# Optimization experiments

Measured on AMD Instinct MI355X. Metric: run time of the kernel, lower is better.

The kernel has to match this reference:

```python
import jax, jax.numpy as jnp
import numpy as np
import math

B, S, E, R = 128, 16, 512, 500  # batch, seq_len, emb_size, relation_num


def setup_inputs() -> dict:
    key = jax.random.key(0)
    ks = jax.random.split(key, 12)
    s = 1.0 / math.sqrt(E)
    emb = jax.random.normal(ks[0], (R + 1, E), jnp.float32) * s
    emb = emb.at[R].set(0.0)  # padding_idx row is zero in torch
    w_ih = jax.random.normal(ks[1], (4 * E, E), jnp.float32) * s
    w_hh = jax.random.normal(ks[2], (4 * E, E), jnp.float32) * s
    b_ih = jax.random.normal(ks[3], (4 * E,), jnp.float32) * s
    b_hh = jax.random.normal(ks[4], (4 * E,), jnp.float32) * s
    fc_w = jax.random.normal(ks[5], (1, E), jnp.float32) * s
    fc_b = jax.random.normal(ks[6], (1,), jnp.float32) * s
    fcq_w = jax.random.normal(ks[7], (E, E), jnp.float32) * s
    fcq_b = jax.random.normal(ks[8], (E,), jnp.float32) * s
    fck_w = jax.random.normal(ks[9], (E, E), jnp.float32) * s
    fck_b = jax.random.normal(ks[10], (E,), jnp.float32) * s
    tokens = jax.random.randint(ks[11], (B, S), 0, R)  # avoid padding idx R
    return dict(tokens=tokens, emb=emb, w_ih=w_ih, w_hh=w_hh, b_ih=b_ih,
                b_hh=b_hh, fc_w=fc_w, fc_b=fc_b, fcq_w=fcq_w, fcq_b=fcq_b,
                fck_w=fck_w, fck_b=fck_b)


def _lstm_pair(x, w_ih, w_hh, b):
    # x: [..., 2, E]; 2-step LSTM from zero state, return final hidden [..., E]
    def cell(xt, h, c):
        g = xt @ w_ih.T + h @ w_hh.T + b
        i, f, gg, o = jnp.split(g, 4, axis=-1)  # torch gate order i,f,g,o
        c = jax.nn.sigmoid(f) * c + jax.nn.sigmoid(i) * jnp.tanh(gg)
        return jax.nn.sigmoid(o) * jnp.tanh(c), c
    z = jnp.zeros_like(x[..., 0, :])
    h1, c1 = cell(x[..., 0, :], z, z)
    h2, _ = cell(x[..., 1, :], h1, c1)
    return h2


def _attention(x, rel_emb, fcq_w, fcq_b, fck_w, fck_b):
    # x: [B,q,E]; keys = [relation embeddings ; x] -> scores [B,q,R+q]
    b = x.shape[0]
    rel = jnp.broadcast_to(rel_emb[None], (b,) + rel_emb.shape)
    kin = jnp.concatenate([rel, x], axis=1)
    k = kin @ fck_w.T + fck_b
    q = x @ fcq_w.T + fcq_b
    return jnp.einsum('bqe,bke->bqk', q, k) / math.sqrt(E)


def _entropy(scores):
    lp = jax.nn.log_softmax(scores, axis=-1)
    return -jnp.sum(jnp.exp(lp) * lp, axis=-1)


def reference(tokens, emb, w_ih, w_hh, b_ih, b_hh, fc_w, fc_b,
              fcq_w, fcq_b, fck_w, fck_b):
    b_lstm = b_ih + b_hh
    rel_emb = emb[:R]  # relation embeddings used as attention keys/values
    cur = emb[tokens]  # [B,S,E]
    bidx = jnp.arange(B)
    losses = []
    for L in range(S, 1, -1):  # lengths processed: S, S-1, ..., 2
        if L > 2:
            # all adjacent pairs, batched 2-step LSTM: [B, L-1, E]
            pairs = jnp.stack([cur[:, :-1], cur[:, 1:]], axis=2)
            h = _lstm_pair(pairs, w_ih, w_hh, b_lstm)
            sc = jax.nn.sigmoid(h @ fc_w.T + fc_b)[..., 0]  # [B, L-1]
            sel = jnp.argmax(sc, axis=-1)  # [B]
            selected = jnp.take_along_axis(h, sel[:, None, None], axis=1)  # [B,1,E]
            scores = _attention(selected, rel_emb, fcq_w, fcq_b, fck_w, fck_b)
            losses.append(_entropy(scores))  # [B,1]
            # weightedAverage: mask is all-False for seq_len==1, plain softmax
            prob = jax.nn.softmax(scores, axis=-1)  # [B,1,R+1]
            all_emb = jnp.concatenate(
                [jnp.broadcast_to(rel_emb[None], (B, R, E)), selected], axis=1)
            merged = jnp.einsum('bqk,bke->bqe', prob, all_emb)[:, 0]  # [B,E]
            # output = inputs.detach().clone(); write merged at sel; drop row sel+1
            base = jax.lax.stop_gradient(cur)
            base = base.at[bidx, sel].set(merged)
            j = jnp.arange(L - 1)[None, :]
            src = j + (j > sel[:, None]).astype(j.dtype)
            cur = jnp.take_along_axis(base, src[:, :, None], axis=1)  # [B,L-1,E]
        else:  # L == 2: plain LSTM over the two tokens
            h = _lstm_pair(cur, w_ih, w_hh, b_lstm)  # [B,E]
            cur = h[:, None, :]
            losses.append(jnp.zeros((B, 1), cur.dtype))
    scores_f = _attention(cur, rel_emb, fcq_w, fcq_b, fck_w, fck_b)  # [B,1,R+1]
    losses.append(_entropy(scores_f))
    loss_tensor = jnp.concatenate(losses, axis=-1)  # [B,S]
    return scores_f[:, 0], loss_tensor
```

## Files before the change

### kernel.cpp

```cpp
#include <hip/hip_runtime.h>
#include <hip/hip_bf16.h>

#define BB 128
#define SS 16
#define EE 512
#define RR 500
#define G4 2048
#define OUT0 64128
#define NSC 501
#define NPAIR 2047
#define NSU 1012

__device__ __forceinline__ float sigm(float x) { return 1.f / (1.f + expf(-x)); }

__device__ float g_blstm[G4];
__device__ float g_blstmr[G4];
__device__ float g_wihr[G4 * EE];
__device__ float g_whhr[G4 * EE];
__device__ float g_fcw[EE + 4];
__device__ float g_qbias[1024];
__device__ float g_Krel[RR * EE];
__device__ float g_cur[BB * SS * EE];
__device__ float g_G[BB * SS * G4];
__device__ float g_h1[BB * SS * EE];
__device__ float g_c1[BB * SS * EE];
__device__ float g_h2[BB * SS * EE];
__device__ float g_sc[BB * SS];
__device__ float g_ent[BB * SS];
__device__ int   g_sel[BB];
__device__ int   g_ord[BB * SS];
__device__ float g_fckwT[EE * EE];
__device__ float g_W2[RR * EE];
__device__ float g_Mx[EE * EE];
__device__ float g_c2[RR + 4];
__device__ float g_v1[EE];
__device__ float g_c0[1];
__device__ float g_su[BB * NSU];

__global__ void k_prep(const float* __restrict__ bih, const float* __restrict__ bhh,
                       const float* __restrict__ fcwv, const float* __restrict__ fcbv,
                       const float* __restrict__ fcqb, const float* __restrict__ fckb) {
    int i = blockIdx.x * blockDim.x + threadIdx.x;
    if (i < G4) g_blstm[i] = bih[i] + bhh[i];
    if (i < EE) {
        g_fcw[i] = fcwv[i];
        g_qbias[i] = fcqb[i];
        g_qbias[EE + i] = fckb[i];
    }
    if (i == 0) g_fcw[EE] = fcbv[0];
    if (i < BB * SS) g_ord[i] = i;
}

__global__ void k_reord(const float* __restrict__ wih, const float* __restrict__ whh) {
    int i = blockIdx.x * blockDim.x + threadIdx.x;
    if (i >= G4 * EE) return;
    int n = i >> 9;
    int k = i & (EE - 1);
    int e = n & (EE - 1);
    int gate = n >> 9;
    int np = 4 * e + gate;
    g_wihr[(size_t)np * EE + k] = wih[i];
    g_whhr[(size_t)np * EE + k] = whh[i];
    if (k == 0) g_blstmr[np] = g_blstm[n];
}

__global__ void k_gather(const int* __restrict__ tok, const float* __restrict__ emb) {
    int i = blockIdx.x * blockDim.x + threadIdx.x;
    if (i >= BB * SS * EE) return;
    int e = i & (EE - 1);
    int r = i >> 9;
    int t = tok[r];
    g_cur[i] = emb[(size_t)t * EE + e];
}

__global__ void k_tr(const float* __restrict__ fckw) {
    int i = blockIdx.x * blockDim.x + threadIdx.x;
    if (i >= EE * EE) return;
    int ep = i >> 9;
    int f = i & (EE - 1);
    g_fckwT[(size_t)f * EE + ep] = fckw[(size_t)ep * EE + f];
}

__global__ __launch_bounds__(512) void k_vprep(const float* __restrict__ fcqw, const float* __restrict__ fckw) {
    __shared__ float sh[512];
    int t = threadIdx.x;
    int blk = blockIdx.x;
    if (blk == 0) {
        float acc = 0.f;
        for (int ep = 0; ep < EE; ep++)
            acc += g_qbias[ep] * fckw[(size_t)ep * EE + t] + g_qbias[EE + ep] * fcqw[(size_t)ep * EE + t];
        g_v1[t] = acc;
    } else if (blk == 1) {
        sh[t] = g_qbias[t] * g_qbias[EE + t];
        __syncthreads();
        for (int s = 256; s > 0; s >>= 1) { if (t < s) sh[t] += sh[t + s]; __syncthreads(); }
        if (t == 0) g_c0[0] = sh[0];
    } else {
        int k = blk - 2;
        sh[t] = g_Krel[(size_t)k * EE + t] * g_qbias[t];
        __syncthreads();
        for (int s = 256; s > 0; s >>= 1) { if (t < s) sh[t] += sh[t + s]; __syncthreads(); }
        if (t == 0) g_c2[k] = sh[0];
    }
}

#define TM 32
#define TN 64
#define TK 32
__device__ __forceinline__ void gemm_dev(
    const float* __restrict__ A, int lda,
    const float* __restrict__ W, int ldw, int wtrans,
    const float* __restrict__ bias, const float* __restrict__ Dadd, int ldd,
    float* __restrict__ C, int ldc, int M, int N, int K)
{
    __shared__ __align__(16) float As[TK][TM + 2];
    __shared__ __align__(16) float Ws[TK][TN + 4];
    int tid = threadIdx.x;
    int mt = blockIdx.y * TM;
    int nt = blockIdx.x * TN;
    int tr = tid >> 4;
    int tc = tid & 15;
    float acc[2][4] = {{0.f,0.f,0.f,0.f},{0.f,0.f,0.f,0.f}};

    int ea = tid * 4;
    int ra = ea >> 5;
    int ka = ea & 31;
    int gmA = mt + ra;
    bool rokA = gmA < M;
    int ew = tid * 8;
    int rw = ew >> 5;
    int kw = ew & 31;
    int gnW = nt + rw;
    bool rokW = gnW < N;

    for (int kt = 0; kt < K; kt += TK) {
        #pragma unroll
        for (int i = 0; i < 4; i++) {
            int gk = kt + ka + i;
            float v = 0.f;
            if (rokA && gk < K) v = A[(size_t)gmA * lda + gk];
            As[ka + i][ra] = v;
        }
        #pragma unroll
        for (int i = 0; i < 8; i++) {
            int gk = kt + kw + i;
            float v = 0.f;
            if (rokW && gk < K)
                v = wtrans ? W[(size_t)gk * ldw + gnW] : W[(size_t)gnW * ldw + gk];
            Ws[kw + i][rw] = v;
        }
        __syncthreads();
        #pragma unroll
        for (int kk = 0; kk < TK; kk++) {
            const float2 a = *(const float2*)&As[kk][2 * tr];
            const float4 w = *(const float4*)&Ws[kk][4 * tc];
            acc[0][0] += a.x * w.x; acc[0][1] += a.x * w.y; acc[0][2] += a.x * w.z; acc[0][3] += a.x * w.w;
            acc[1][0] += a.y * w.x; acc[1][1] += a.y * w.y; acc[1][2] += a.y * w.z; acc[1][3] += a.y * w.w;
        }
        __syncthreads();
    }
    #pragma unroll
    for (int i = 0; i < 2; i++) {
        int gm = mt + 2 * tr + i;
        if (gm >= M) continue;
        #pragma unroll
        for (int j = 0; j < 4; j++) {
            int gn = nt + 4 * tc + j;
            if (gn >= N) continue;
            float v = (i == 0) ? ((j == 0) ? acc[0][0] : (j == 1) ? acc[0][1] : (j == 2) ? acc[0][2] : acc[0][3])
                               : ((j == 0) ? acc[1][0] : (j == 1) ? acc[1][1] : (j == 2) ? acc[1][2] : acc[1][3]);
            if (bias) v += bias[gn];
            if (Dadd) v += Dadd[(size_t)gm * ldd + gn];
            C[(size_t)gm * ldc + gn] = v;
        }
    }
}

#define UM 128
#define UN 128
#define UK 32
template<int MODE>
__global__ __launch_bounds__(256) void kg_bigF() {
    __shared__ __align__(16) float As[UK][UM + 4];
    __shared__ __align__(16) float Ws[UK][UN + 4];
    const float* __restrict__ A = (MODE == 0) ? g_cur : g_h1;
    const float* __restrict__ W = (MODE == 0) ? g_wihr : g_whhr;
    const int M = (MODE == 0) ? (BB * SS) : NPAIR;
    int tid = threadIdx.x;
    int mt = blockIdx.y * UM;
    int nt = blockIdx.x * UN;
    int tr = tid >> 4;
    int tc = tid & 15;
    float acc[8][8] = {};

    int ra = tid & 127;
    int ka = (tid >> 7) << 4;
    int gmA = mt + ra;
    bool rokA = gmA < M;
    const float* Arow = A + (size_t)(rokA ? gmA : 0) * EE;
    const float* Wrow = W + (size_t)(nt + ra) * EE;

    float4 pa[4] = {{0,0,0,0},{0,0,0,0},{0,0,0,0},{0,0,0,0}};
    float4 pw[4];
    #pragma unroll
    for (int j = 0; j < 4; j++) {
        if (rokA) pa[j] = *(const float4*)&Arow[ka + 4 * j];
        pw[j] = *(const float4*)&Wrow[ka + 4 * j];
    }

    for (int kt = 0; kt < EE; kt += UK) {
        __syncthreads();
        #pragma unroll
        for (int j = 0; j < 4; j++) {
            As[ka + 4 * j + 0][ra] = pa[j].x;
            As[ka + 4 * j + 1][ra] = pa[j].y;
            As[ka + 4 * j + 2][ra] = pa[j].z;
            As[ka + 4 * j + 3][ra] = pa[j].w;
            Ws[ka + 4 * j + 0][ra] = pw[j].x;
            Ws[ka + 4 * j + 1][ra] = pw[j].y;
            Ws[ka + 4 * j + 2][ra] = pw[j].z;
            Ws[ka + 4 * j + 3][ra] = pw[j].w;
        }
        __syncthreads();
        if (kt + UK < EE) {
            int k2 = kt + UK + ka;
            #pragma unroll
            for (int j = 0; j < 4; j++) {
                if (rokA) pa[j] = *(const float4*)&Arow[k2 + 4 * j];
                pw[j] = *(const float4*)&Wrow[k2 + 4 * j];
            }
        }
        #pragma unroll
        for (int kk = 0; kk < UK; kk++) {
            const float4 aA = *(const float4*)&As[kk][4 * tr];
            const float4 aB = *(const float4*)&As[kk][64 + 4 * tr];
            const float4 wA = *(const float4*)&Ws[kk][4 * tc];
            const float4 wB = *(const float4*)&Ws[kk][64 + 4 * tc];
            const float am[8] = {aA.x, aA.y, aA.z, aA.w, aB.x, aB.y, aB.z, aB.w};
            const float wn[8] = {wA.x, wA.y, wA.z, wA.w, wB.x, wB.y, wB.z, wB.w};
            #pragma unroll
            for (int i = 0; i < 8; i++)
                #pragma unroll
                for (int j = 0; j < 8; j++)
                    acc[i][j] += am[i] * wn[j];
        }
    }

    int c0 = nt + 4 * tc;
    int c1c = c0 + 64;
    int e0 = (nt >> 2) + tc;
    #pragma unroll
    for (int ri = 0; ri < 8; ri++) {
        int row = (ri < 4) ? (4 * tr + ri) : (60 + 4 * tr + ri);
        int gm = mt + row;
        if (gm >= M) continue;
        float q0x = acc[ri][0], q0y = acc[ri][1], q0z = acc[ri][2], q0w = acc[ri][3];
        float q1x = acc[ri][4], q1y = acc[ri][5], q1z = acc[ri][6], q1w = acc[ri][7];
        if (MODE == 0) {
            const float4 b0 = *(const float4*)&g_blstmr[c0];
            const float4 b1 = *(const float4*)&g_blstmr[c1c];
            q0x += b0.x; q0y += b0.y; q0z += b0.z; q0w += b0.w;
            q1x += b1.x; q1y += b1.y; q1z += b1.z; q1w += b1.w;
            float4 o0 = {q0x, q0y, q0z, q0w};
            float4 o1 = {q1x, q1y, q1z, q1w};
            *(float4*)&g_G[(size_t)gm * G4 + c0]  = o0;
            *(float4*)&g_G[(size_t)gm * G4 + c1c] = o1;
            float cA = sigm(q0x) * tanhf(q0z);
            g_c1[(size_t)gm * EE + e0] = cA;
            g_h1[(size_t)gm * EE + e0] = sigm(q0w) * tanhf(cA);
            float cB = sigm(q1x) * tanhf(q1z);
            g_c1[(size_t)gm * EE + e0 + 16] = cB;
            g_h1[(size_t)gm * EE + e0 + 16] = sigm(q1w) * tanhf(cB);
        } else {
            const float4 d0 = *(const float4*)&g_G[(size_t)(gm + 1) * G4 + c0];
            const float4 d1 = *(const float4*)&g_G[(size_t)(gm + 1) * G4 + c1c];
            q0x += d0.x; q0y += d0.y; q0z += d0.z; q0w += d0.w;
            q1x += d1.x; q1y += d1.y; q1z += d1.z; q1w += d1.w;
            float c1a = g_c1[(size_t)gm * EE + e0];
            float c1b = g_c1[(size_t)gm * EE + e0 + 16];
            float cA = sigm(q0y) * c1a + sigm(q0x) * tanhf(q0z);
            g_h2[(size_t)gm * EE + e0] = sigm(q0w) * tanhf(cA);
            float cB = sigm(q1y) * c1b + sigm(q1x) * tanhf(q1z);
            g_h2[(size_t)gm * EE + e0 + 16] = sigm(q1w) * tanhf(cB);
        }
    }
}

__global__ __launch_bounds__(256) void kg_Krel(const float* __restrict__ emb, const float* __restrict__ fckw) {
    gemm_dev(emb, EE, fckw, EE, 0, g_qbias + EE, nullptr, 0, g_Krel, EE, RR, EE, EE);
}
__global__ __launch_bounds__(256) void kg_W2(const float* __restrict__ fcqw) {
    gemm_dev(g_Krel, EE, fcqw, EE, 1, nullptr, nullptr, 0, g_W2, EE, RR, EE, EE);
}
__global__ __launch_bounds__(256) void kg_Mx(const float* __restrict__ fcqw) {
    gemm_dev(g_fckwT, EE, fcqw, EE, 1, nullptr, nullptr, 0, g_Mx, EE, EE, EE, EE);
}

__global__ __launch_bounds__(256) void k_scI() {
    int m = blockIdx.x;
    int t = threadIdx.x;
    __shared__ float red[256];
    const float* h = g_h2 + (size_t)m * EE;
    float part = h[t] * g_fcw[t] + h[t + 256] * g_fcw[t + 256];
    red[t] = part;
    __syncthreads();
    for (int s = 128; s > 0; s >>= 1) { if (t < s) red[t] += red[t + s]; __syncthreads(); }
    if (t == 0) g_sc[m] = red[0];
}

__global__ __launch_bounds__(256) void k_scP(int L) {
    int m = blockIdx.x;
    int b = m >> 1;
    int tcand = m & 1;
    int s = g_sel[b];
    int p = s - 1 + tcand;
    bool valid = tcand == 0 ? (s >= 1) : (s <= L - 3);
    if (!valid) return;
    int physL = g_ord[b * SS + p];
    int t = threadIdx.x;
    __shared__ float red[256];
    const float* h = g_h2 + (size_t)physL * EE;
    float part = h[t] * g_fcw[t] + h[t + 256] * g_fcw[t + 256];
    red[t] = part;
    __syncthreads();
    for (int s2 = 128; s2 > 0; s2 >>= 1) { if (t < s2) red[t] += red[t + s2]; __syncthreads(); }
    if (t == 0) g_sc[b * SS + p] = red[0];
}

__global__ __launch_bounds__(256) void kg_su(int P) {
    __shared__ __align__(16) float As[TK][TM + 2];
    __shared__ __align__(16) float Ws[TK][TN + 4];
    __shared__ int s_phys[TM];
    int tid = threadIdx.x;
    int mt = blockIdx.y * TM;
    int nt = blockIdx.x * TN;
    int tr = tid >> 4;
    int tc = tid & 15;
    float acc[2][4] = {{0.f,0.f,0.f,0.f},{0.f,0.f,0.f,0.f}};

    if (tid < TM) {
        int b = mt + tid;
        float best = -1e30f; int bi = 0;
        for (int p = 0; p < P; p++) {
            float v = g_sc[b * SS + p];
            if (v > best) { best = v; bi = p; }
        }
        s_phys[tid] = g_ord[b * SS + bi];
        if (blockIdx.x == 0) g_sel[b] = bi;
    }
    __syncthreads();

    int ea = tid * 4;
    int ra = ea >> 5;
    int ka = ea & 31;
    int physA = s_phys[ra];
    int ew = tid * 8;
    int rw = ew >> 5;
    int kw = ew & 31;
    int gnW = nt + rw;
    bool rokW = gnW < NSU;
    const float* Wrow = nullptr;
    if (rokW) Wrow = (gnW < RR) ? (g_W2 + (size_t)gnW * EE) : (g_Mx + (size_t)(gnW - RR) * EE);

    for (int kt = 0; kt < EE; kt += TK) {
        #pragma unroll
        for (int i = 0; i < 4; i++)
            As[ka + i][ra] = g_h2[(size_t)physA * EE + kt + ka + i];
        #pragma unroll
        for (int i = 0; i < 8; i++)
            Ws[kw + i][rw] = rokW ? Wrow[kt + kw + i] : 0.f;
        __syncthreads();
        #pragma unroll
        for (int kk = 0; kk < TK; kk++) {
            const float2 a = *(const float2*)&As[kk][2 * tr];
            const float4 w = *(const float4*)&Ws[kk][4 * tc];
            acc[0][0] += a.x * w.x; acc[0][1] += a.x * w.y; acc[0][2] += a.x * w.z; acc[0][3] += a.x * w.w;
            acc[1][0] += a.y * w.x; acc[1][1] += a.y * w.y; acc[1][2] += a.y * w.z; acc[1][3] += a.y * w.w;
        }
        __syncthreads();
    }
    #pragma unroll
    for (int i = 0; i < 2; i++) {
        int gm = mt + 2 * tr + i;
        #pragma unroll
        for (int j = 0; j < 4; j++) {
            int gn = nt + 4 * tc + j;
            if (gn >= NSU) continue;
            float v = (i == 0) ? ((j == 0) ? acc[0][0] : (j == 1) ? acc[0][1] : (j == 2) ? acc[0][2] : acc[0][3])
                               : ((j == 0) ? acc[1][0] : (j == 1) ? acc[1][1] : (j == 2) ? acc[1][2] : acc[1][3]);
            g_su[(size_t)gm * NSU + gn] = v + (gn < RR ? g_c2[gn] : 0.f);
        }
    }
}

__global__ __launch_bounds__(256) void kg_GiF() {
    __shared__ __align__(16) float As[TK][TM + 2];
    __shared__ __align__(16) float Ws[TK][TN + 4];
    __shared__ int s_phys[TM];
    int tid = threadIdx.x;
    int mt = blockIdx.y * TM;
    int nt = blockIdx.x * TN;
    int tr = tid >> 4;
    int tc = tid & 15;
    float acc[2][4] = {{0.f,0.f,0.f,0.f},{0.f,0.f,0.f,0.f}};

    if (tid < TM) {
        int b = mt + tid;
        s_phys[tid] = g_ord[b * SS + g_sel[b]];
    }
    __syncthreads();

    int ea = tid * 4;
    int ra = ea >> 5;
    int ka = ea & 31;
    int physA = s_phys[ra];
    int ew = tid * 8;
    int rw = ew >> 5;
    int kw = ew & 31;
    int gnW = nt + rw;

    for (int kt = 0; kt < EE; kt += TK) {
        #pragma unroll
        for (int i = 0; i < 4; i++)
            As[ka + i][ra] = g_cur[(size_t)physA * EE + kt + ka + i];
        #pragma unroll
        for (int i = 0; i < 8; i++)
            Ws[kw + i][rw] = g_wihr[(size_t)gnW * EE + kt + kw + i];
        __syncthreads();
        #pragma unroll
        for (int kk = 0; kk < TK; kk++) {
            const float2 a = *(const float2*)&As[kk][2 * tr];
            const float4 w = *(const float4*)&Ws[kk][4 * tc];
            acc[0][0] += a.x * w.x; acc[0][1] += a.x * w.y; acc[0][2] += a.x * w.z; acc[0][3] += a.x * w.w;
            acc[1][0] += a.y * w.x; acc[1][1] += a.y * w.y; acc[1][2] += a.y * w.z; acc[1][3] += a.y * w.w;
        }
        __syncthreads();
    }
    int c0 = nt + 4 * tc;
    int e0 = (nt >> 2) + tc;
    const float4 b4 = *(const float4*)&g_blstmr[c0];
    #pragma unroll
    for (int i = 0; i < 2; i++) {
        int phys = s_phys[2 * tr + i];
        float qx = acc[i][0] + b4.x;
        float qy = acc[i][1] + b4.y;
        float qz = acc[i][2] + b4.z;
        float qw = acc[i][3] + b4.w;
        float4 o = {qx, qy, qz, qw};
        *(float4*)&g_G[(size_t)phys * G4 + c0] = o;
        float cA = sigm(qx) * tanhf(qz);
        g_c1[(size_t)phys * EE + e0] = cA;
        g_h1[(size_t)phys * EE + e0] = sigm(qw) * tanhf(cA);
    }
}

__global__ __launch_bounds__(256) void kg_g2iF(int L) {
    __shared__ __align__(16) float As[TK][TM + 2];
    __shared__ __align__(16) float Ws[TK][TN + 4];
    __shared__ int s_physA[TM];
    __shared__ int s_physD[TM];
    __shared__ int s_val[TM];
    int tid = threadIdx.x;
    int mt = blockIdx.y * TM;
    int nt = blockIdx.x * TN;
    int tr = tid >> 4;
    int tc = tid & 15;
    float acc[2][4] = {{0.f,0.f,0.f,0.f},{0.f,0.f,0.f,0.f}};

    if (tid < TM) {
        int gm = mt + tid;
        int b = gm >> 1;
        int tcand = gm & 1;
        int s = g_sel[b];
        int p = min(max(s - 1 + tcand, 0), 14);
        s_physA[tid] = g_ord[b * SS + p];
        s_physD[tid] = g_ord[b * SS + p + 1];
        s_val[tid] = tcand == 0 ? (s >= 1) : (s <= L - 3);
    }
    __syncthreads();

    int ea = tid * 4;
    int ra = ea >> 5;
    int ka = ea & 31;
    int physA = s_physA[ra];
    int ew = tid * 8;
    int rw = ew >> 5;
    int kw = ew & 31;
    int gnW = nt + rw;

    for (int kt = 0; kt < EE; kt += TK) {
        #pragma unroll
        for (int i = 0; i < 4; i++)
            As[ka + i][ra] = g_h1[(size_t)physA * EE + kt + ka + i];
        #pragma unroll
        for (int i = 0; i < 8; i++)
            Ws[kw + i][rw] = g_whhr[(size_t)gnW * EE + kt + kw + i];
        __syncthreads();
        #pragma unroll
        for (int kk = 0; kk < TK; kk++) {
            const float2 a = *(const float2*)&As[kk][2 * tr];
            const float4 w = *(const float4*)&Ws[kk][4 * tc];
            acc[0][0] += a.x * w.x; acc[0][1] += a.x * w.y; acc[0][2] += a.x * w.z; acc[0][3] += a.x * w.w;
            acc[1][0] += a.y * w.x; acc[1][1] += a.y * w.y; acc[1][2] += a.y * w.z; acc[1][3] += a.y * w.w;
        }
        __syncthreads();
    }
    int c0 = nt + 4 * tc;
    int e0 = (nt >> 2) + tc;
    #pragma unroll
    for (int i = 0; i < 2; i++) {
        int r = 2 * tr + i;
        if (!s_val[r]) continue;
        int pA = s_physA[r];
        int pD = s_physD[r];
        const float4 d4 = *(const float4*)&g_G[(size_t)pD * G4 + c0];
        float qx = acc[i][0] + d4.x;
        float qy = acc[i][1] + d4.y;
        float qz = acc[i][2] + d4.z;
        float qw = acc[i][3] + d4.w;
        float c1v = g_c1[(size_t)pA * EE + e0];
        float cA = sigm(qy) * c1v + sigm(qx) * tanhf(qz);
        g_h2[(size_t)pA * EE + e0] = sigm(qw) * tanhf(cA);
    }
}

__global__ __launch_bounds__(512) void k_smu(int col, int finalFlag, int L,
                                             const float* __restrict__ emb, float* __restrict__ out) {
    int b = blockIdx.x;
    int t = threadIdx.x;
    __shared__ float sh[512];
    __shared__ float srow[NSC];
    __shared__ float s_p500;
    const float* su = g_su + (size_t)b * NSU;
    int s = g_sel[b];
    int phys = g_ord[b * SS + s];
    const float* h2row = g_h2 + (size_t)phys * EE;
    const float isq = 0.044194173824159216f;

    float hv = h2row[t];
    sh[t] = hv * (su[RR + t] + g_v1[t]);
    __syncthreads();
    for (int ss = 256; ss > 0; ss >>= 1) { if (t < ss) sh[t] += sh[t + ss]; __syncthreads(); }
    if (t == 0) srow[RR] = (sh[0] + g_c0[0]) * isq;
    __syncthreads();
    if (t < RR) srow[t] = su[t] * isq;
    __syncthreads();
    float mx = (t < NSC) ? srow[t] : -1e30f;
    sh[t] = mx; __syncthreads();
    for (int ss = 256; ss > 0; ss >>= 1) { if (t < ss) sh[t] = fmaxf(sh[t], sh[t + ss]); __syncthreads(); }
    mx = sh[0]; __syncthreads();
    float zp = (t < NSC) ? expf(srow[t] - mx) : 0.f;
    sh[t] = zp; __syncthreads();
    for (int ss = 256; ss > 0; ss >>= 1) { if (t < ss) sh[t] += sh[t + ss]; __syncthreads(); }
    float lse = mx + logf(sh[0]);
    __syncthreads();
    float p = (t < NSC) ? expf(srow[t] - lse) : 0.f;
    float ep = (t < NSC) ? p * (lse - srow[t]) : 0.f;
    if (finalFlag && t < NSC) out[(size_t)b * NSC + t] = srow[t];
    sh[t] = ep; __syncthreads();
    for (int ss = 256; ss > 0; ss >>= 1) { if (t < ss) sh[t] += sh[t + ss]; __syncthreads(); }
    if (finalFlag) {
        if (t < 16) {
            float v = (t == 15) ? sh[0] : ((t == 14) ? 0.f : g_ent[b * SS + t]);
            out[OUT0 + b * 16 + t] = v;
        }
        return;
    }
    if (t == 0) g_ent[b * SS + col] = sh[0];

    __syncthreads();
    if (t < NSC) srow[t] = p;
    if (t == RR) s_p500 = p;
    __syncthreads();
    float macc = 0.f;
    #pragma unroll 4
    for (int k = 0; k < RR; k++) macc += srow[k] * emb[(size_t)k * EE + t];
    g_cur[(size_t)phys * EE + t] = macc + s_p500 * hv;
    if (t == 0) {
        for (int j = s + 1; j <= L - 2; j++) g_ord[b * SS + j] = g_ord[b * SS + j + 1];
        for (int pp = s + 1; pp <= L - 3; pp++) g_sc[b * SS + pp] = g_sc[b * SS + pp + 1];
    }
}

extern "C" void kernel_launch(void* const* d_in, const int* in_sizes, int n_in,
                              void* d_out, int out_size, void* d_ws, size_t ws_size,
                              hipStream_t stream) {
    const int*   tokens = (const int*)d_in[0];
    const float* emb    = (const float*)d_in[1];
    const float* wih    = (const float*)d_in[2];
    const float* whh    = (const float*)d_in[3];
    const float* bih    = (const float*)d_in[4];
    const float* bhh    = (const float*)d_in[5];
    const float* fcwv   = (const float*)d_in[6];
    const float* fcbv   = (const float*)d_in[7];
    const float* fcqw   = (const float*)d_in[8];
    const float* fcqb   = (const float*)d_in[9];
    const float* fckw   = (const float*)d_in[10];
    const float* fckb   = (const float*)d_in[11];
    float* out = (float*)d_out;

    auto grid32 = [](int M, int N) { return dim3((unsigned)((N + TN - 1) / TN), (unsigned)((M + TM - 1) / TM)); };

    k_prep<<<dim3(8), dim3(256), 0, stream>>>(bih, bhh, fcwv, fcbv, fcqb, fckb);
    k_reord<<<dim3((G4 * EE) / 256), dim3(256), 0, stream>>>(wih, whh);
    kg_Krel<<<grid32(RR, EE), dim3(256), 0, stream>>>(emb, fckw);
    k_tr<<<dim3((EE * EE + 255) / 256), dim3(256), 0, stream>>>(fckw);
    kg_W2<<<grid32(RR, EE), dim3(256), 0, stream>>>(fcqw);
    kg_Mx<<<grid32(EE, EE), dim3(256), 0, stream>>>(fcqw);
    k_vprep<<<dim3(502), dim3(512), 0, stream>>>(fcqw, fckw);
    k_gather<<<dim3((BB * SS * EE + 255) / 256), dim3(256), 0, stream>>>(tokens, emb);

    kg_bigF<0><<<dim3(16, 16), dim3(256), 0, stream>>>();
    kg_bigF<1><<<dim3(16, 16), dim3(256), 0, stream>>>();
    k_scI<<<dim3(NPAIR), dim3(256), 0, stream>>>();

    for (int L = SS; L >= 3; L--) {
        kg_su<<<grid32(BB, NSU), dim3(256), 0, stream>>>(L - 1);
        k_smu<<<dim3(BB), dim3(512), 0, stream>>>(SS - L, 0, L, emb, out);
        kg_GiF<<<grid32(BB, G4), dim3(256), 0, stream>>>();
        kg_g2iF<<<grid32(2 * BB, G4), dim3(256), 0, stream>>>(L);
        k_scP<<<dim3(2 * BB), dim3(256), 0, stream>>>(L);
    }

    kg_su<<<grid32(BB, NSU), dim3(256), 0, stream>>>(1);
    k_smu<<<dim3(BB), dim3(512), 0, stream>>>(15, 1, 2, emb, out);

    (void)in_sizes; (void)n_in; (void)out_size; (void)d_ws; (void)ws_size;
}
```

Before: 1.953 ms.

## Fuse per-step score GEMM and pair scoring into softmax-merge kernel; split-K big LSTM GEMMs

The per-iteration kg_su GEMM and the k_scP pair-score kernel are removed. Their work is folded into k_smu, which now computes the neighbor pair scores, the argmax selection, and a GEMV against a pre-transposed concatenated weight matrix (g_T) on its own. The two big LSTM GEMMs are split along K into two z-slices that write partial buffers, followed by separate elementwise epilogue kernels, to fill more of the GPU. This cuts two launches per loop step and intermediate traffic, but k_smu now uses only 128 blocks for a 512x1024 GEMV per row, and the split-K adds partial-buffer reads and writes.

Result: slower. 2.196 ms (+12.4%).

```diff
diff --git a/kernel.cpp b/kernel.cpp
--- a/kernel.cpp
+++ b/kernel.cpp
@@ -9,7 +9,6 @@
 #define OUT0 64128
 #define NSC 501
 #define NPAIR 2047
-#define NSU 1012
 
 __device__ __forceinline__ float sigm(float x) { return 1.f / (1.f + expf(-x)); }
 
@@ -29,13 +28,15 @@
 __device__ float g_ent[BB * SS];
 __device__ int   g_sel[BB];
 __device__ int   g_ord[BB * SS];
+__device__ float g_P0[BB * SS * G4];
+__device__ float g_P1[BB * SS * G4];
 __device__ float g_fckwT[EE * EE];
 __device__ float g_W2[RR * EE];
 __device__ float g_Mx[EE * EE];
+__device__ float g_T[EE * 1024];
 __device__ float g_c2[RR + 4];
 __device__ float g_v1[EE];
 __device__ float g_c0[1];
-__device__ float g_su[BB * NSU];
 
 __global__ void k_prep(const float* __restrict__ bih, const float* __restrict__ bhh,
                        const float* __restrict__ fcwv, const float* __restrict__ fcbv,
@@ -79,6 +80,26 @@
     int ep = i >> 9;
     int f = i & (EE - 1);
     g_fckwT[(size_t)f * EE + ep] = fckw[(size_t)ep * EE + f];
+}
+
+__global__ __launch_bounds__(256) void k_trT() {
+    __shared__ float tile[32][33];
+    int jt = blockIdx.x * 32;
+    int kt = blockIdx.y * 32;
+    int tx = threadIdx.x & 31;
+    int ty = threadIdx.x >> 5;
+    #pragma unroll
+    for (int r = 0; r < 4; r++) {
+        int j = jt + ty + 8 * r;
+        float v = 0.f;
+        if (j < 512) v = g_Mx[(size_t)j * EE + kt + tx];
+        else if (j < 1012) v = g_W2[(size_t)(j - 512) * EE + kt + tx];
+        tile[ty + 8 * r][tx] = v;
+    }
+    __syncthreads();
+    #pragma unroll
+    for (int r = 0; r < 4; r++)
+        g_T[(size_t)(kt + ty + 8 * r) * 1024 + jt + tx] = tile[tx][ty + 8 * r];
 }
 
 __global__ __launch_bounds__(512) void k_vprep(const float* __restrict__ fcqw, const float* __restrict__ fckw) {
@@ -180,12 +201,14 @@
 #define UN 128
 #define UK 32
 template<int MODE>
-__global__ __launch_bounds__(256) void kg_bigF() {
+__global__ __launch_bounds__(256) void kg_bigP() {
     __shared__ __align__(16) float As[UK][UM + 4];
     __shared__ __align__(16) float Ws[UK][UN + 4];
     const float* __restrict__ A = (MODE == 0) ? g_cur : g_h1;
-    const float* __restrict__ W = (MODE == 0) ? g_wihr : g_whhr;
+    const float* __restrict__ Wm = (MODE == 0) ? g_wihr : g_whhr;
     const int M = (MODE == 0) ? (BB * SS) : NPAIR;
+    float* __restrict__ P = (blockIdx.z == 0) ? g_P0 : g_P1;
+    const int kbase = blockIdx.z * (EE / 2);
     int tid = threadIdx.x;
     int mt = blockIdx.y * UM;
     int nt = blockIdx.x * UN;
@@ -197,10 +220,10 @@
     int ka = (tid >> 7) << 4;
     int gmA = mt + ra;
     bool rokA = gmA < M;
-    const float* Arow = A + (size_t)(rokA ? gmA : 0) * EE;
-    const float* Wrow = W + (size_t)(nt + ra) * EE;
-
-    float4 pa[4] = {{0,0,0,0},{0,0,0,0},{0,0,0,0},{0,0,0,0}};
+    const float* Arow = A + (size_t)(rokA ? gmA : 0) * EE + kbase;
+    const float* Wrow = Wm + (size_t)(nt + ra) * EE + kbase;
+
+    float4 pa[4] = {};
     float4 pw[4];
     #pragma unroll
     for (int j = 0; j < 4; j++) {
@@ -208,7 +231,7 @@
         pw[j] = *(const float4*)&Wrow[ka + 4 * j];
     }
 
-    for (int kt = 0; kt < EE; kt += UK) {
+    for (int kt = 0; kt < EE / 2; kt += UK) {
         __syncthreads();
         #pragma unroll
         for (int j = 0; j < 4; j++) {
@@ -222,7 +245,7 @@
             Ws[ka + 4 * j + 3][ra] = pw[j].w;
         }
         __syncthreads();
-        if (kt + UK < EE) {
+        if (kt + UK < EE / 2) {
             int k2 = kt + UK + ka;
             #pragma unroll
             for (int j = 0; j < 4; j++) {
@@ -248,42 +271,54 @@
 
     int c0 = nt + 4 * tc;
     int c1c = c0 + 64;
-    int e0 = (nt >> 2) + tc;
     #pragma unroll
     for (int ri = 0; ri < 8; ri++) {
         int row = (ri < 4) ? (4 * tr + ri) : (60 + 4 * tr + ri);
         int gm = mt + row;
         if (gm >= M) continue;
-        float q0x = acc[ri][0], q0y = acc[ri][1], q0z = acc[ri][2], q0w = acc[ri][3];
-        float q1x = acc[ri][4], q1y = acc[ri][5], q1z = acc[ri][6], q1w = acc[ri][7];
-        if (MODE == 0) {
-            const float4 b0 = *(const float4*)&g_blstmr[c0];
-            const float4 b1 = *(const float4*)&g_blstmr[c1c];
-            q0x += b0.x; q0y += b0.y; q0z += b0.z; q0w += b0.w;
-            q1x += b1.x; q1y += b1.y; q1z += b1.z; q1w += b1.w;
-            float4 o0 = {q0x, q0y, q0z, q0w};
-            float4 o1 = {q1x, q1y, q1z, q1w};
-            *(float4*)&g_G[(size_t)gm * G4 + c0]  = o0;
-            *(float4*)&g_G[(size_t)gm * G4 + c1c] = o1;
-            float cA = sigm(q0x) * tanhf(q0z);
-            g_c1[(size_t)gm * EE + e0] = cA;
-            g_h1[(size_t)gm * EE + e0] = sigm(q0w) * tanhf(cA);
-            float cB = sigm(q1x) * tanhf(q1z);
-            g_c1[(size_t)gm * EE + e0 + 16] = cB;
-            g_h1[(size_t)gm * EE + e0 + 16] = sigm(q1w) * tanhf(cB);
-        } else {
-            const float4 d0 = *(const float4*)&g_G[(size_t)(gm + 1) * G4 + c0];
-            const float4 d1 = *(const float4*)&g_G[(size_t)(gm + 1) * G4 + c1c];
-            q0x += d0.x; q0y += d0.y; q0z += d0.z; q0w += d0.w;
-            q1x += d1.x; q1y += d1.y; q1z += d1.z; q1w += d1.w;
-            float c1a = g_c1[(size_t)gm * EE + e0];
-            float c1b = g_c1[(size_t)gm * EE + e0 + 16];
-            float cA = sigm(q0y) * c1a + sigm(q0x) * tanhf(q0z);
-            g_h2[(size_t)gm * EE + e0] = sigm(q0w) * tanhf(cA);
-            float cB = sigm(q1y) * c1b + sigm(q1x) * tanhf(q1z);
-            g_h2[(size_t)gm * EE + e0 + 16] = sigm(q1w) * tanhf(cB);
-        }
-    }
+        float4 o0 = {acc[ri][0], acc[ri][1], acc[ri][2], acc[ri][3]};
+        float4 o1 = {acc[ri][4], acc[ri][5], acc[ri][6], acc[ri][7]};
+        *(float4*)&P[(size_t)gm * G4 + c0]  = o0;
+        *(float4*)&P[(size_t)gm * G4 + c1c] = o1;
+    }
+}
+
+__global__ void k_ep0() {
+    int idx = blockIdx.x * blockDim.x + threadIdx.x;
+    if (idx >= BB * SS * EE) return;
+    int m = idx >> 9;
+    int e = idx & (EE - 1);
+    int c0 = 4 * e;
+    const float4 p0 = *(const float4*)&g_P0[(size_t)m * G4 + c0];
+    const float4 p1 = *(const float4*)&g_P1[(size_t)m * G4 + c0];
+    const float4 b4 = *(const float4*)&g_blstmr[c0];
+    float qx = p0.x + p1.x + b4.x;
+    float qy = p0.y + p1.y + b4.y;
+    float qz = p0.z + p1.z + b4.z;
+    float qw = p0.w + p1.w + b4.w;
+    float4 o = {qx, qy, qz, qw};
+    *(float4*)&g_G[(size_t)m * G4 + c0] = o;
+    float cA = sigm(qx) * tanhf(qz);
+    g_c1[idx] = cA;
+    g_h1[idx] = sigm(qw) * tanhf(cA);
+}
+
+__global__ void k_ep1() {
+    int idx = blockIdx.x * blockDim.x + threadIdx.x;
+    if (idx >= NPAIR * EE) return;
+    int m = idx >> 9;
+    int e = idx & (EE - 1);
+    int c0 = 4 * e;
+    const float4 p0 = *(const float4*)&g_P0[(size_t)m * G4 + c0];
+    const float4 p1 = *(const float4*)&g_P1[(size_t)m * G4 + c0];
+    const float4 d4 = *(const float4*)&g_G[(size_t)(m + 1) * G4 + c0];
+    float qx = p0.x + p1.x + d4.x;
+    float qy = p0.y + p1.y + d4.y;
+    float qz = p0.z + p1.z + d4.z;
+    float qw = p0.w + p1.w + d4.w;
+    float c1v = g_c1[(size_t)m * EE + e];
+    float cA = sigm(qy) * c1v + sigm(qx) * tanhf(qz);
+    g_h2[(size_t)m * EE + e] = sigm(qw) * tanhf(cA);
 }
 
 __global__ __launch_bounds__(256) void kg_Krel(const float* __restrict__ emb, const float* __restrict__ fckw) {
@@ -306,91 +341,6 @@
     __syncthreads();
     for (int s = 128; s > 0; s >>= 1) { if (t < s) red[t] += red[t + s]; __syncthreads(); }
     if (t == 0) g_sc[m] = red[0];
-}
-
-__global__ __launch_bounds__(256) void k_scP(int L) {
-    int m = blockIdx.x;
-    int b = m >> 1;
-    int tcand = m & 1;
-    int s = g_sel[b];
-    int p = s - 1 + tcand;
-    bool valid = tcand == 0 ? (s >= 1) : (s <= L - 3);
-    if (!valid) return;
-    int physL = g_ord[b * SS + p];
-    int t = threadIdx.x;
-    __shared__ float red[256];
-    const float* h = g_h2 + (size_t)physL * EE;
-    float part = h[t] * g_fcw[t] + h[t + 256] * g_fcw[t + 256];
-    red[t] = part;
-    __syncthreads();
-    for (int s2 = 128; s2 > 0; s2 >>= 1) { if (t < s2) red[t] += red[t + s2]; __syncthreads(); }
-    if (t == 0) g_sc[b * SS + p] = red[0];
-}
-
-__global__ __launch_bounds__(256) void kg_su(int P) {
-    __shared__ __align__(16) float As[TK][TM + 2];
-    __shared__ __align__(16) float Ws[TK][TN + 4];
-    __shared__ int s_phys[TM];
-    int tid = threadIdx.x;
-    int mt = blockIdx.y * TM;
-    int nt = blockIdx.x * TN;
-    int tr = tid >> 4;
-    int tc = tid & 15;
-    float acc[2][4] = {{0.f,0.f,0.f,0.f},{0.f,0.f,0.f,0.f}};
-
-    if (tid < TM) {
-        int b = mt + tid;
-        float best = -1e30f; int bi = 0;
-        for (int p = 0; p < P; p++) {
-            float v = g_sc[b * SS + p];
-            if (v > best) { best = v; bi = p; }
-        }
-        s_phys[tid] = g_ord[b * SS + bi];
-        if (blockIdx.x == 0) g_sel[b] = bi;
-    }
-    __syncthreads();
-
-    int ea = tid * 4;
-    int ra = ea >> 5;
-    int ka = ea & 31;
-    int physA = s_phys[ra];
-    int ew = tid * 8;
-    int rw = ew >> 5;
-    int kw = ew & 31;
-    int gnW = nt + rw;
-    bool rokW = gnW < NSU;
-    const float* Wrow = nullptr;
-    if (rokW) Wrow = (gnW < RR) ? (g_W2 + (size_t)gnW * EE) : (g_Mx + (size_t)(gnW - RR) * EE);
-
-    for (int kt = 0; kt < EE; kt += TK) {
-        #pragma unroll
-        for (int i = 0; i < 4; i++)
-            As[ka + i][ra] = g_h2[(size_t)physA * EE + kt + ka + i];
-        #pragma unroll
-        for (int i = 0; i < 8; i++)
-            Ws[kw + i][rw] = rokW ? Wrow[kt + kw + i] : 0.f;
-        __syncthreads();
-        #pragma unroll
-        for (int kk = 0; kk < TK; kk++) {
-            const float2 a = *(const float2*)&As[kk][2 * tr];
-            const float4 w = *(const float4*)&Ws[kk][4 * tc];
-            acc[0][0] += a.x * w.x; acc[0][1] += a.x * w.y; acc[0][2] += a.x * w.z; acc[0][3] += a.x * w.w;
-            acc[1][0] += a.y * w.x; acc[1][1] += a.y * w.y; acc[1][2] += a.y * w.z; acc[1][3] += a.y * w.w;
-        }
-        __syncthreads();
-    }
-    #pragma unroll
-    for (int i = 0; i < 2; i++) {
-        int gm = mt + 2 * tr + i;
-        #pragma unroll
-        for (int j = 0; j < 4; j++) {
-            int gn = nt + 4 * tc + j;
-            if (gn >= NSU) continue;
-            float v = (i == 0) ? ((j == 0) ? acc[0][0] : (j == 1) ? acc[0][1] : (j == 2) ? acc[0][2] : acc[0][3])
-                               : ((j == 0) ? acc[1][0] : (j == 1) ? acc[1][1] : (j == 2) ? acc[1][2] : acc[1][3]);
-            g_su[(size_t)gm * NSU + gn] = v + (gn < RR ? g_c2[gn] : 0.f);
-        }
-    }
 }
 
 __global__ __launch_bounds__(256) void kg_GiF() {
@@ -524,26 +474,74 @@
     }
 }
 
-__global__ __launch_bounds__(512) void k_smu(int col, int finalFlag, int L,
+__global__ __launch_bounds__(512) void k_smu(int col, int finalFlag, int L, int firstFlag,
                                              const float* __restrict__ emb, float* __restrict__ out) {
     int b = blockIdx.x;
     int t = threadIdx.x;
     __shared__ float sh[512];
     __shared__ float srow[NSC];
+    __shared__ float h2s[512];
+    __shared__ float scl[SS];
+    __shared__ int   ordl[SS];
+    __shared__ int   s_seli, s_physi;
     __shared__ float s_p500;
-    const float* su = g_su + (size_t)b * NSU;
-    int s = g_sel[b];
-    int phys = g_ord[b * SS + s];
+
+    if (t < SS) { scl[t] = g_sc[b * SS + t]; ordl[t] = g_ord[b * SS + t]; }
+    __syncthreads();
+
+    if (!firstFlag && !finalFlag) {
+        int sp = g_sel[b];
+        #pragma unroll
+        for (int c = 0; c < 2; c++) {
+            bool valid = (c == 0) ? (sp >= 1) : (sp <= L - 2);
+            int p = sp - 1 + c;
+            if (valid) {
+                const float* h = g_h2 + (size_t)ordl[p] * EE;
+                if (t < 256) sh[t] = h[t] * g_fcw[t] + h[t + 256] * g_fcw[t + 256];
+            }
+            __syncthreads();
+            if (valid) {
+                for (int s2 = 128; s2 > 0; s2 >>= 1) {
+                    if (t < s2) sh[t] += sh[t + s2];
+                    __syncthreads();
+                }
+                if (t == 0) scl[p] = sh[0];
+            }
+            __syncthreads();
+        }
+    }
+
+    if (t == 0) {
+        float best = -1e30f; int bi = 0;
+        int P = L - 1;
+        for (int p = 0; p < P; p++) { float v = scl[p]; if (v > best) { best = v; bi = p; } }
+        s_seli = bi;
+        s_physi = ordl[bi];
+        g_sel[b] = bi;
+    }
+    __syncthreads();
+    int s = s_seli;
+    int phys = s_physi;
     const float* h2row = g_h2 + (size_t)phys * EE;
+    float hv = h2row[t];
+    h2s[t] = hv;
+    __syncthreads();
+
+    float acc0 = 0.f, acc1 = 0.f;
+    #pragma unroll 4
+    for (int k = 0; k < EE; k++) {
+        float hk = h2s[k];
+        acc0 += hk * g_T[(k << 10) + t];
+        acc1 += hk * g_T[(k << 10) + 512 + t];
+    }
+
     const float isq = 0.044194173824159216f;
-
-    float hv = h2row[t];
-    sh[t] = hv * (su[RR + t] + g_v1[t]);
+    sh[t] = hv * (acc0 + g_v1[t]);
     __syncthreads();
     for (int ss = 256; ss > 0; ss >>= 1) { if (t < ss) sh[t] += sh[t + ss]; __syncthreads(); }
     if (t == 0) srow[RR] = (sh[0] + g_c0[0]) * isq;
     __syncthreads();
-    if (t < RR) srow[t] = su[t] * isq;
+    if (t < RR) srow[t] = (acc1 + g_c2[t]) * isq;
     __syncthreads();
     float mx = (t < NSC) ? srow[t] : -1e30f;
     sh[t] = mx; __syncthreads();
@@ -554,8 +552,8 @@
     for (int ss = 256; ss > 0; ss >>= 1) { if (t < ss) sh[t] += sh[t + ss]; __syncthreads(); }
     float lse = mx + logf(sh[0]);
     __syncthreads();
-    float p = (t < NSC) ? expf(srow[t] - lse) : 0.f;
-    float ep = (t < NSC) ? p * (lse - srow[t]) : 0.f;
+    float pb = (t < NSC) ? expf(srow[t] - lse) : 0.f;
+    float ep = (t < NSC) ? pb * (lse - srow[t]) : 0.f;
     if (finalFlag && t < NSC) out[(size_t)b * NSC + t] = srow[t];
     sh[t] = ep; __syncthreads();
     for (int ss = 256; ss > 0; ss >>= 1) { if (t < ss) sh[t] += sh[t + ss]; __syncthreads(); }
@@ -569,17 +567,19 @@
     if (t == 0) g_ent[b * SS + col] = sh[0];
 
     __syncthreads();
-    if (t < NSC) srow[t] = p;
-    if (t == RR) s_p500 = p;
+    if (t < NSC) srow[t] = pb;
+    if (t == RR) s_p500 = pb;
     __syncthreads();
     float macc = 0.f;
     #pragma unroll 4
     for (int k = 0; k < RR; k++) macc += srow[k] * emb[(size_t)k * EE + t];
     g_cur[(size_t)phys * EE + t] = macc + s_p500 * hv;
     if (t == 0) {
-        for (int j = s + 1; j <= L - 2; j++) g_ord[b * SS + j] = g_ord[b * SS + j + 1];
-        for (int pp = s + 1; pp <= L - 3; pp++) g_sc[b * SS + pp] = g_sc[b * SS + pp + 1];
-    }
+        for (int j = s + 1; j <= L - 2; j++) ordl[j] = ordl[j + 1];
+        for (int pp = s + 1; pp <= L - 3; pp++) scl[pp] = scl[pp + 1];
+    }
+    __syncthreads();
+    if (t < SS) { g_ord[b * SS + t] = ordl[t]; g_sc[b * SS + t] = scl[t]; }
 }
 
 extern "C" void kernel_launch(void* const* d_in, const int* in_sizes, int n_in,
@@ -607,23 +607,23 @@
     k_tr<<<dim3((EE * EE + 255) / 256), dim3(256), 0, stream>>>(fckw);
     kg_W2<<<grid32(RR, EE), dim3(256), 0, stream>>>(fcqw);
     kg_Mx<<<grid32(EE, EE), dim3(256), 0, stream>>>(fcqw);
+    k_trT<<<dim3(32, 16), dim3(256), 0, stream>>>();
     k_vprep<<<dim3(502), dim3(512), 0, stream>>>(fcqw, fckw);
     k_gather<<<dim3((BB * SS * EE + 255) / 256), dim3(256), 0, stream>>>(tokens, emb);
 
-    kg_bigF<0><<<dim3(16, 16), dim3(256), 0, stream>>>();
-    kg_bigF<1><<<dim3(16, 16), dim3(256), 0, stream>>>();
+    kg_bigP<0><<<dim3(16, 16, 2), dim3(256), 0, stream>>>();
+    k_ep0<<<dim3((BB * SS * EE) / 256), dim3(256), 0, stream>>>();
+    kg_bigP<1><<<dim3(16, 16, 2), dim3(256), 0, stream>>>();
+    k_ep1<<<dim3((NPAIR * EE + 255) / 256), dim3(256), 0, stream>>>();
     k_scI<<<dim3(NPAIR), dim3(256), 0, stream>>>();
 
     for (int L = SS; L >= 3; L--) {
-        kg_su<<<grid32(BB, NSU), dim3(256), 0, stream>>>(L - 1);
-        k_smu<<<dim3(BB), dim3(512), 0, stream>>>(SS - L, 0, L, emb, out);
+        k_smu<<<dim3(BB), dim3(512), 0, stream>>>(SS - L, 0, L, L == SS ? 1 : 0, emb, out);
         kg_GiF<<<grid32(BB, G4), dim3(256), 0, stream>>>();
         kg_g2iF<<<grid32(2 * BB, G4), dim3(256), 0, stream>>>(L);
-        k_scP<<<dim3(2 * BB), dim3(256), 0, stream>>>(L);
-    }
-
-    kg_su<<<grid32(BB, NSU), dim3(256), 0, stream>>>(1);
-    k_smu<<<dim3(BB), dim3(512), 0, stream>>>(15, 1, 2, emb, out);
+    }
+
+    k_smu<<<dim3(BB), dim3(512), 0, stream>>>(15, 1, 2, 0, emb, out);
 
     (void)in_sizes; (void)n_in; (void)out_size; (void)d_ws; (void)ws_size;
 }
```

## Fuse score projection into LSTM step-2 GEMM epilogue via last-block reduction

Applied to the files above, without the earlier changes.

Removes the separate k_scP launch from each of the 14 loop iterations. The fc dot product is now computed in the kg_g2iF epilogue: each block writes per-row partial sums, and the last block in each row tile (found with an atomic counter) reduces them into g_sc. It also pre-transposes fcq_w so the W2 and Mx precompute GEMMs use the non-transposed operand mode. The cost is extra shared-memory partials, a threadfence, an atomic per block, and a serial 32-way reduction done by the last block.

Measured after the change: 2.281 ms. 16.8% more time.

```diff
diff --git a/kernel.cpp b/kernel.cpp
--- a/kernel.cpp
+++ b/kernel.cpp
@@ -29,7 +29,10 @@
 __device__ float g_ent[BB * SS];
 __device__ int   g_sel[BB];
 __device__ int   g_ord[BB * SS];
+__device__ float g_scPart[2 * BB * 32];
+__device__ int   g_cnt[8];
 __device__ float g_fckwT[EE * EE];
+__device__ float g_fcqwT[EE * EE];
 __device__ float g_W2[RR * EE];
 __device__ float g_Mx[EE * EE];
 __device__ float g_c2[RR + 4];
@@ -49,6 +52,7 @@
     }
     if (i == 0) g_fcw[EE] = fcbv[0];
     if (i < BB * SS) g_ord[i] = i;
+    if (i < 8) g_cnt[i] = 0;
 }
 
 __global__ void k_reord(const float* __restrict__ wih, const float* __restrict__ whh) {
@@ -73,12 +77,13 @@
     g_cur[i] = emb[(size_t)t * EE + e];
 }
 
-__global__ void k_tr(const float* __restrict__ fckw) {
+__global__ void k_tr(const float* __restrict__ fckw, const float* __restrict__ fcqw) {
     int i = blockIdx.x * blockDim.x + threadIdx.x;
     if (i >= EE * EE) return;
     int ep = i >> 9;
     int f = i & (EE - 1);
     g_fckwT[(size_t)f * EE + ep] = fckw[(size_t)ep * EE + f];
+    g_fcqwT[(size_t)f * EE + ep] = fcqw[(size_t)ep * EE + f];
 }
 
 __global__ __launch_bounds__(512) void k_vprep(const float* __restrict__ fcqw, const float* __restrict__ fckw) {
@@ -200,7 +205,7 @@
     const float* Arow = A + (size_t)(rokA ? gmA : 0) * EE;
     const float* Wrow = W + (size_t)(nt + ra) * EE;
 
-    float4 pa[4] = {{0,0,0,0},{0,0,0,0},{0,0,0,0},{0,0,0,0}};
+    float4 pa[4] = {};
     float4 pw[4];
     #pragma unroll
     for (int j = 0; j < 4; j++) {
@@ -289,11 +294,11 @@
 __global__ __launch_bounds__(256) void kg_Krel(const float* __restrict__ emb, const float* __restrict__ fckw) {
     gemm_dev(emb, EE, fckw, EE, 0, g_qbias + EE, nullptr, 0, g_Krel, EE, RR, EE, EE);
 }
-__global__ __launch_bounds__(256) void kg_W2(const float* __restrict__ fcqw) {
-    gemm_dev(g_Krel, EE, fcqw, EE, 1, nullptr, nullptr, 0, g_W2, EE, RR, EE, EE);
-}
-__global__ __launch_bounds__(256) void kg_Mx(const float* __restrict__ fcqw) {
-    gemm_dev(g_fckwT, EE, fcqw, EE, 1, nullptr, nullptr, 0, g_Mx, EE, EE, EE, EE);
+__global__ __launch_bounds__(256) void kg_W2() {
+    gemm_dev(g_Krel, EE, g_fcqwT, EE, 0, nullptr, nullptr, 0, g_W2, EE, RR, EE, EE);
+}
+__global__ __launch_bounds__(256) void kg_Mx() {
+    gemm_dev(g_fckwT, EE, g_fcqwT, EE, 0, nullptr, nullptr, 0, g_Mx, EE, EE, EE, EE);
 }
 
 __global__ __launch_bounds__(256) void k_scI() {
@@ -306,25 +311,6 @@
     __syncthreads();
     for (int s = 128; s > 0; s >>= 1) { if (t < s) red[t] += red[t + s]; __syncthreads(); }
     if (t == 0) g_sc[m] = red[0];
-}
-
-__global__ __launch_bounds__(256) void k_scP(int L) {
-    int m = blockIdx.x;
-    int b = m >> 1;
-    int tcand = m & 1;
-    int s = g_sel[b];
-    int p = s - 1 + tcand;
-    bool valid = tcand == 0 ? (s >= 1) : (s <= L - 3);
-    if (!valid) return;
-    int physL = g_ord[b * SS + p];
-    int t = threadIdx.x;
-    __shared__ float red[256];
-    const float* h = g_h2 + (size_t)physL * EE;
-    float part = h[t] * g_fcw[t] + h[t + 256] * g_fcw[t + 256];
-    red[t] = part;
-    __syncthreads();
-    for (int s2 = 128; s2 > 0; s2 >>= 1) { if (t < s2) red[t] += red[t + s2]; __syncthreads(); }
-    if (t == 0) g_sc[b * SS + p] = red[0];
 }
 
 __global__ __launch_bounds__(256) void kg_su(int P) {
@@ -460,6 +446,8 @@
     __shared__ int s_physA[TM];
     __shared__ int s_physD[TM];
     __shared__ int s_val[TM];
+    __shared__ float s_part[TM][17];
+    __shared__ int s_last;
     int tid = threadIdx.x;
     int mt = blockIdx.y * TM;
     int nt = blockIdx.x * TN;
@@ -507,20 +495,50 @@
     }
     int c0 = nt + 4 * tc;
     int e0 = (nt >> 2) + tc;
+    float fw = g_fcw[e0];
     #pragma unroll
     for (int i = 0; i < 2; i++) {
         int r = 2 * tr + i;
-        if (!s_val[r]) continue;
-        int pA = s_physA[r];
-        int pD = s_physD[r];
-        const float4 d4 = *(const float4*)&g_G[(size_t)pD * G4 + c0];
-        float qx = acc[i][0] + d4.x;
-        float qy = acc[i][1] + d4.y;
-        float qz = acc[i][2] + d4.z;
-        float qw = acc[i][3] + d4.w;
-        float c1v = g_c1[(size_t)pA * EE + e0];
-        float cA = sigm(qy) * c1v + sigm(qx) * tanhf(qz);
-        g_h2[(size_t)pA * EE + e0] = sigm(qw) * tanhf(cA);
+        float h2v = 0.f;
+        if (s_val[r]) {
+            int pA = s_physA[r];
+            int pD = s_physD[r];
+            const float4 d4 = *(const float4*)&g_G[(size_t)pD * G4 + c0];
+            float qx = acc[i][0] + d4.x;
+            float qy = acc[i][1] + d4.y;
+            float qz = acc[i][2] + d4.z;
+            float qw = acc[i][3] + d4.w;
+            float c1v = g_c1[(size_t)pA * EE + e0];
+            float cA = sigm(qy) * c1v + sigm(qx) * tanhf(qz);
+            h2v = sigm(qw) * tanhf(cA);
+            g_h2[(size_t)pA * EE + e0] = h2v;
+        }
+        s_part[r][tc] = h2v * fw;
+    }
+    __syncthreads();
+
+    if (tid < TM && s_val[tid]) {
+        float sum = 0.f;
+        #pragma unroll
+        for (int j = 0; j < 16; j++) sum += s_part[tid][j];
+        g_scPart[(mt + tid) * 32 + blockIdx.x] = sum;
+    }
+    __threadfence();
+    __syncthreads();
+    if (tid == 0) s_last = (atomicAdd(&g_cnt[blockIdx.y], 1) == 31);
+    __syncthreads();
+    if (s_last) {
+        __threadfence();
+        if (tid < TM && s_val[tid]) {
+            int gm = mt + tid;
+            float tot = 0.f;
+            for (int bx = 0; bx < 32; bx++) tot += g_scPart[gm * 32 + bx];
+            int b = gm >> 1;
+            int tcand = gm & 1;
+            int p = g_sel[b] - 1 + tcand;
+            g_sc[b * SS + p] = tot;
+        }
+        if (tid == 0) g_cnt[blockIdx.y] = 0;
     }
 }
 
@@ -554,8 +572,8 @@
     for (int ss = 256; ss > 0; ss >>= 1) { if (t < ss) sh[t] += sh[t + ss]; __syncthreads(); }
     float lse = mx + logf(sh[0]);
     __syncthreads();
-    float p = (t < NSC) ? expf(srow[t] - lse) : 0.f;
-    float ep = (t < NSC) ? p * (lse - srow[t]) : 0.f;
+    float pb = (t < NSC) ? expf(srow[t] - lse) : 0.f;
+    float ep = (t < NSC) ? pb * (lse - srow[t]) : 0.f;
     if (finalFlag && t < NSC) out[(size_t)b * NSC + t] = srow[t];
     sh[t] = ep; __syncthreads();
     for (int ss = 256; ss > 0; ss >>= 1) { if (t < ss) sh[t] += sh[t + ss]; __syncthreads(); }
@@ -569,8 +587,8 @@
     if (t == 0) g_ent[b * SS + col] = sh[0];
 
     __syncthreads();
-    if (t < NSC) srow[t] = p;
-    if (t == RR) s_p500 = p;
+    if (t < NSC) srow[t] = pb;
+    if (t == RR) s_p500 = pb;
     __syncthreads();
     float macc = 0.f;
     #pragma unroll 4
@@ -604,9 +622,9 @@
     k_prep<<<dim3(8), dim3(256), 0, stream>>>(bih, bhh, fcwv, fcbv, fcqb, fckb);
     k_reord<<<dim3((G4 * EE) / 256), dim3(256), 0, stream>>>(wih, whh);
     kg_Krel<<<grid32(RR, EE), dim3(256), 0, stream>>>(emb, fckw);
-    k_tr<<<dim3((EE * EE + 255) / 256), dim3(256), 0, stream>>>(fckw);
-    kg_W2<<<grid32(RR, EE), dim3(256), 0, stream>>>(fcqw);
-    kg_Mx<<<grid32(EE, EE), dim3(256), 0, stream>>>(fcqw);
+    k_tr<<<dim3((EE * EE + 255) / 256), dim3(256), 0, stream>>>(fckw, fcqw);
+    kg_W2<<<grid32(RR, EE), dim3(256), 0, stream>>>();
+    kg_Mx<<<grid32(EE, EE), dim3(256), 0, stream>>>();
     k_vprep<<<dim3(502), dim3(512), 0, stream>>>(fcqw, fckw);
     k_gather<<<dim3((BB * SS * EE + 255) / 256), dim3(256), 0, stream>>>(tokens, emb);
 
@@ -619,7 +637,6 @@
         k_smu<<<dim3(BB), dim3(512), 0, stream>>>(SS - L, 0, L, emb, out);
         kg_GiF<<<grid32(BB, G4), dim3(256), 0, stream>>>();
         kg_g2iF<<<grid32(2 * BB, G4), dim3(256), 0, stream>>>(L);
-        k_scP<<<dim3(2 * BB), dim3(256), 0, stream>>>(L);
     }
 
     kg_su<<<grid32(BB, NSU), dim3(256), 0, stream>>>(1);
```
